# Optimization experiments

Hardware: AMD Instinct MI355X
Metric: run time of the kernel (lower is better)

The kernel has to match this reference:

```python
import jax, jax.numpy as jnp
import numpy as np

N_NODES = 100000
N_EDGES = 1_600_000
IN_C, HID_C, CLS_C = 128, 256, 64


def setup_inputs() -> dict:
    key = jax.random.key(0)
    ks = jax.random.split(key, 8)
    x = jax.random.normal(ks[0], (N_NODES, IN_C), dtype=jnp.float32)
    edge_index = jax.random.randint(ks[1], (2, N_EDGES), 0, N_NODES, dtype=jnp.int64)
    s1 = 1.0 / np.sqrt(IN_C)
    s2 = 1.0 / np.sqrt(HID_C)
    W1l = jax.random.uniform(ks[2], (IN_C, HID_C), jnp.float32, -s1, s1)
    W1r = jax.random.uniform(ks[3], (IN_C, HID_C), jnp.float32, -s1, s1)
    b1 = jnp.zeros((HID_C,), jnp.float32)
    W2l = jax.random.uniform(ks[4], (HID_C, CLS_C), jnp.float32, -s2, s2)
    W2r = jax.random.uniform(ks[5], (HID_C, CLS_C), jnp.float32, -s2, s2)
    b2 = jnp.zeros((CLS_C,), jnp.float32)
    return {"x": x, "edge_index": edge_index,
            "W1l": W1l, "W1r": W1r, "b1": b1,
            "W2l": W2l, "W2r": W2r, "b2": b2}


def _sage_conv(x, src, dst, Wl, Wr, b, num_nodes):
    # mean aggregation of source features onto destination nodes
    agg = jax.ops.segment_sum(x[src], dst, num_segments=num_nodes)  # [N, F]
    deg = jax.ops.segment_sum(jnp.ones((src.shape[0], 1), x.dtype), dst,
                              num_segments=num_nodes)               # [N, 1]
    agg = agg / jnp.maximum(deg, 1.0)  # zero-degree nodes -> 0
    return agg @ Wl + x @ Wr + b


def reference(x, edge_index, W1l, W1r, b1, W2l, W2r, b2):
    src, dst = edge_index[0], edge_index[1]
    n = x.shape[0]
    h = jax.nn.relu(_sage_conv(x, src, dst, W1l, W1r, b1, n))
    # dropout(p=0.5) is identity in eval mode
    out = _sage_conv(h, src, dst, W2l, W2r, b2, n)
    return jax.nn.sigmoid(out)
```

## Files before the change

kernel.cpp:

```cpp
#include <hip/hip_runtime.h>

typedef __attribute__((ext_vector_type(8))) short short8;
typedef __attribute__((ext_vector_type(4))) float floatx4;
typedef __attribute__((ext_vector_type(2))) float floatx2;

static __device__ __forceinline__ unsigned short f2bf(float f) {
  unsigned int u = __builtin_bit_cast(unsigned int, f);
  u += 0x7FFFu + ((u >> 16) & 1u);
  return (unsigned short)(u >> 16);
}
static __device__ __forceinline__ float bf2f(unsigned short s) {
  unsigned int u = ((unsigned int)s) << 16;
  return __builtin_bit_cast(float, u);
}
static __device__ __forceinline__ unsigned int pk4_fp8(float a, float b, float c, float d) {
  int lo = __builtin_amdgcn_cvt_pk_fp8_f32(a, b, 0, false);
  int hi = __builtin_amdgcn_cvt_pk_fp8_f32(c, d, 0, false);
  return (unsigned int)((lo & 0xffff) | ((hi & 0xffff) << 16));
}
static __device__ __forceinline__ floatx4 unpk4_fp8(unsigned int p) {
  floatx2 lo = __builtin_amdgcn_cvt_pk_f32_fp8((int)p, false);
  floatx2 hi = __builtin_amdgcn_cvt_pk_f32_fp8((int)p, true);
  floatx4 r = {lo.x, lo.y, hi.x, hi.y};
  return r;
}

#define NBUCK 512
#define BIN_CHUNK 8192


__global__ __launch_bounds__(256) void bhist(const int* __restrict__ dst,
                                             int* __restrict__ bcnt, int E) {
  __shared__ int h[NBUCK];
  for (int i = threadIdx.x; i < NBUCK; i += 256) h[i] = 0;
  __syncthreads();
  int stride = gridDim.x * 256;
  for (int i = blockIdx.x * 256 + threadIdx.x; i < E; i += stride)
    atomicAdd(&h[dst[i] >> 8], 1);
  __syncthreads();
  for (int i = threadIdx.x; i < NBUCK; i += 256)
    if (h[i]) atomicAdd(&bcnt[i], h[i]);
}

__global__ __launch_bounds__(256) void bscan(const int* __restrict__ bcnt,
                                             int* __restrict__ bbase,
                                             int* __restrict__ bcur,
                                             int* __restrict__ rs, int N, int E) {
  __shared__ int ps[256];
  int t = threadIdx.x;
  int v0 = bcnt[2 * t], v1 = bcnt[2 * t + 1];
  int tsum = v0 + v1;
  ps[t] = tsum;
  __syncthreads();
  for (int off = 1; off < 256; off <<= 1) {
    int x = (t >= off) ? ps[t - off] : 0;
    __syncthreads();
    ps[t] += x;
    __syncthreads();
  }
  int excl = ps[t] - tsum;
  bbase[2 * t] = excl;     bcur[2 * t] = excl;
  bbase[2 * t + 1] = excl + v0; bcur[2 * t + 1] = excl + v0;
  if (t == 0) rs[N] = E;
}

__global__ __launch_bounds__(256) void binscatter(const int* __restrict__ src,
                                                  const int* __restrict__ dst,
                                                  int* __restrict__ bcur,
                                                  unsigned int* __restrict__ staging,
                                                  int E) {
  __shared__ int h[NBUCK];
  __shared__ int cur[NBUCK];
  for (int i = threadIdx.x; i < NBUCK; i += 256) h[i] = 0;
  __syncthreads();
  int base = blockIdx.x * BIN_CHUNK;
  int end = base + BIN_CHUNK; if (end > E) end = E;
  for (int i = base + threadIdx.x; i < end; i += 256)
    atomicAdd(&h[dst[i] >> 8], 1);
  __syncthreads();
  for (int i = threadIdx.x; i < NBUCK; i += 256)
    cur[i] = h[i] ? atomicAdd(&bcur[i], h[i]) : 0;
  __syncthreads();
  for (int i = base + threadIdx.x; i < end; i += 256) {
    int d = dst[i], s = src[i];
    int b = d >> 8;
    int pos = atomicAdd(&cur[b], 1);
    staging[pos] = ((unsigned int)(d & 255) << 17) | (unsigned int)s;
  }
}

__global__ __launch_bounds__(256) void bucketfinal(const unsigned int* __restrict__ staging,
                                                   const int* __restrict__ bbase,
                                                   const int* __restrict__ bcnt,
                                                   int* __restrict__ rs,
                                                   int* __restrict__ csr_src, int N) {
  int b = blockIdx.x;
  int base = bbase[b], cnt = bcnt[b];
  __shared__ int h[256];
  __shared__ int ps[256];
  __shared__ int cur[256];
  int t = threadIdx.x;
  h[t] = 0;
  __syncthreads();
  for (int i = t; i < cnt; i += 256)
    atomicAdd(&h[staging[base + i] >> 17], 1);
  __syncthreads();
  int hv = h[t];
  ps[t] = hv;
  __syncthreads();
  for (int off = 1; off < 256; off <<= 1) {
    int x = (t >= off) ? ps[t - off] : 0;
    __syncthreads();
    ps[t] += x;
    __syncthreads();
  }
  int run = base + ps[t] - hv;
  int w = (b << 8) + t;
  cur[t] = run;
  if (w < N) rs[w] = run;
  __syncthreads();
  for (int i = t; i < cnt; i += 256) {
    unsigned int v = staging[base + i];
    int pos = atomicAdd(&cur[v >> 17], 1);
    csr_src[pos] = (int)(v & 0x1FFFFu);
  }
}

__global__ void convw(const float* __restrict__ W1l, const float* __restrict__ W1r,
                      const float* __restrict__ W2l, const float* __restrict__ W2r,
                      unsigned short* __restrict__ W1p, unsigned short* __restrict__ W2p) {
  int i = blockIdx.x * blockDim.x + threadIdx.x;
  if (i < 8192) {
    int lane = i & 63, ni = (i >> 6) & 3, kk = (i >> 8) & 7, w = i >> 11;
    int fm = lane & 15, fq = lane >> 4;
    int n = w * 64 + ni * 16 + fm;
    int k0 = kk * 32 + fq * 8;
    unsigned short r[8];
#pragma unroll
    for (int j = 0; j < 8; j++) {
      int k = k0 + j;
      float v = (k < 128) ? W1l[k * 256 + n] : W1r[(k - 128) * 256 + n];
      r[j] = f2bf(v);
    }
    *reinterpret_cast<uint4*>(W1p + (size_t)i * 8) = *reinterpret_cast<uint4*>(r);
  } else if (i < 8192 + 4096) {
    int j2 = i - 8192;
    int lane = j2 & 63, ni = (j2 >> 6) & 1, kk = (j2 >> 7) & 7, w = j2 >> 10;
    int fm = lane & 15, fq = lane >> 4;
    int n = w * 32 + ni * 16 + fm;
    int k0 = kk * 32 + fq * 8;
    unsigned short r[8];
#pragma unroll
    for (int j = 0; j < 8; j++) {
      int k = k0 + j;
      float v = (n < 64) ? W2l[k * 64 + n] : W2r[k * 64 + (n - 64)];
      r[j] = f2bf(v);
    }
    *reinterpret_cast<uint4*>(W2p + (size_t)j2 * 8) = *reinterpret_cast<uint4*>(r);
  }
}

__global__ void convx(const float* __restrict__ x, unsigned short* __restrict__ A1,
                      unsigned int* __restrict__ xq, int n_nodes) {
  int i = blockIdx.x * blockDim.x + threadIdx.x;
  if (i < n_nodes * 32) {
    int node = i >> 5, c4 = (i & 31) * 4;
    float4 v = *reinterpret_cast<const float4*>(x + (size_t)node * 128 + c4);
    unsigned short r[4] = { f2bf(v.x), f2bf(v.y), f2bf(v.z), f2bf(v.w) };
    *reinterpret_cast<uint2*>(A1 + (size_t)node * 256 + 128 + c4) =
        *reinterpret_cast<uint2*>(r);
    xq[node * 32 + (i & 31)] = pk4_fp8(v.x, v.y, v.z, v.w);
  }
}

__global__ __launch_bounds__(256) void agg1_kernel(const int* __restrict__ csr_src,
                                                   const int* __restrict__ rs,
                                                   const uint4* __restrict__ xq,
                                                   unsigned short* __restrict__ A1,
                                                   int n_nodes) {
  int lane = threadIdx.x & 63;
  int wave = threadIdx.x >> 6;
  int grp = lane >> 3;
  int ch4 = lane & 7;
  int w = blockIdx.x * 32 + wave * 8 + grp;
  if (w >= n_nodes) return;
  int e0 = rs[w], e1 = rs[w + 1];
  floatx4 a0[4] = {{0,0,0,0},{0,0,0,0},{0,0,0,0},{0,0,0,0}};
  floatx4 a1[4] = {{0,0,0,0},{0,0,0,0},{0,0,0,0},{0,0,0,0}};
  int e = e0;
  for (; e + 1 < e1; e += 2) {
    uint4 p0 = xq[(csr_src[e] << 3) | ch4];
    uint4 p1 = xq[(csr_src[e + 1] << 3) | ch4];
    a0[0] += unpk4_fp8(p0.x); a0[1] += unpk4_fp8(p0.y);
    a0[2] += unpk4_fp8(p0.z); a0[3] += unpk4_fp8(p0.w);
    a1[0] += unpk4_fp8(p1.x); a1[1] += unpk4_fp8(p1.y);
    a1[2] += unpk4_fp8(p1.z); a1[3] += unpk4_fp8(p1.w);
  }
  if (e < e1) {
    uint4 p = xq[(csr_src[e] << 3) | ch4];
    a0[0] += unpk4_fp8(p.x); a0[1] += unpk4_fp8(p.y);
    a0[2] += unpk4_fp8(p.z); a0[3] += unpk4_fp8(p.w);
  }
  int d = e1 - e0; if (d < 1) d = 1;
  float sc = 1.0f / (float)d;
  unsigned short r[16];
#pragma unroll
  for (int j = 0; j < 4; j++) {
    floatx4 a = a0[j] + a1[j];
    r[4 * j + 0] = f2bf(a.x * sc); r[4 * j + 1] = f2bf(a.y * sc);
    r[4 * j + 2] = f2bf(a.z * sc); r[4 * j + 3] = f2bf(a.w * sc);
  }
  unsigned short* dst = A1 + (size_t)w * 256 + ch4 * 16;
  *reinterpret_cast<uint4*>(dst) = *reinterpret_cast<uint4*>(r);
  *reinterpret_cast<uint4*>(dst + 8) = *reinterpret_cast<uint4*>(r + 8);
}

#define LDSW 264
__global__ __launch_bounds__(256, 4) void gemm_fused(const unsigned short* __restrict__ A1,
                                                     const unsigned short* __restrict__ W1p,
                                                     const unsigned short* __restrict__ W2p,
                                                     const float* __restrict__ b1,
                                                     unsigned char* __restrict__ zq,
                                                     unsigned short* __restrict__ rb,
                                                     int M) {
  __shared__ unsigned short smem[64 * LDSW];
  const int tid = threadIdx.x;
  const int lane = tid & 63;
  const int wave = tid >> 6;
  const int m0 = blockIdx.x * 64;
  const int fm = lane & 15;
  const int fq = lane >> 4;
  const short8* __restrict__ W1v = reinterpret_cast<const short8*>(W1p);
  const short8* __restrict__ W2v = reinterpret_cast<const short8*>(W2p);

#pragma unroll
  for (int j = 0; j < 8; j++) {
    int c = j * 256 + tid;
    int row = c >> 5, ch = c & 31;
    int gr = m0 + row; if (gr >= M) gr = M - 1;
    int4 v = *reinterpret_cast<const int4*>(A1 + (size_t)gr * 256 + ch * 8);
    *reinterpret_cast<int4*>(&smem[row * LDSW + ch * 8]) = v;
  }

  float bb[4];
#pragma unroll
  for (int ni = 0; ni < 4; ni++) bb[ni] = b1[wave * 64 + ni * 16 + fm];

  __syncthreads();

  floatx4 acc1[4][4] = {};
#pragma unroll 2
  for (int kk = 0; kk < 8; kk++) {
    short8 af[4], bfr[4];
#pragma unroll
    for (int mi = 0; mi < 4; mi++)
      af[mi] = *reinterpret_cast<const short8*>(
          &smem[(mi * 16 + fm) * LDSW + kk * 32 + fq * 8]);
#pragma unroll
    for (int ni = 0; ni < 4; ni++)
      bfr[ni] = W1v[((wave * 8 + kk) * 4 + ni) * 64 + lane];
#pragma unroll
    for (int mi = 0; mi < 4; mi++)
#pragma unroll
      for (int ni = 0; ni < 4; ni++)
        acc1[mi][ni] = __builtin_amdgcn_mfma_f32_16x16x32_bf16(af[mi], bfr[ni],
                                                               acc1[mi][ni], 0, 0, 0);
  }

  __syncthreads();

#pragma unroll
  for (int mi = 0; mi < 4; mi++)
#pragma unroll
    for (int ni = 0; ni < 4; ni++)
#pragma unroll
      for (int r = 0; r < 4; r++) {
        float v = acc1[mi][ni][r] + bb[ni];
        v = v > 0.f ? v : 0.f;
        smem[(mi * 16 + fq * 4 + r) * LDSW + wave * 64 + ni * 16 + fm] = f2bf(v);
      }
  __syncthreads();

  floatx4 acc2[4][2] = {};
#pragma unroll 2
  for (int kk = 0; kk < 8; kk++) {
    short8 hf[4], wf[2];
#pragma unroll
    for (int mi = 0; mi < 4; mi++)
      hf[mi] = *reinterpret_cast<const short8*>(
          &smem[(mi * 16 + fm) * LDSW + kk * 32 + fq * 8]);
#pragma unroll
    for (int ni = 0; ni < 2; ni++)
      wf[ni] = W2v[((wave * 8 + kk) * 2 + ni) * 64 + lane];
#pragma unroll
    for (int mi = 0; mi < 4; mi++)
#pragma unroll
      for (int ni = 0; ni < 2; ni++)
        acc2[mi][ni] = __builtin_amdgcn_mfma_f32_16x16x32_bf16(hf[mi], wf[ni],
                                                               acc2[mi][ni], 0, 0, 0);
  }

#pragma unroll
  for (int mi = 0; mi < 4; mi++)
#pragma unroll
    for (int ni = 0; ni < 2; ni++)
#pragma unroll
      for (int r = 0; r < 4; r++) {
        int grow = m0 + mi * 16 + fq * 4 + r;
        if (grow < M) {
          float v = acc2[mi][ni][r];
          int col = (wave & 1) * 32 + ni * 16 + fm;
          if (wave < 2) {
            int b8 = __builtin_amdgcn_cvt_pk_fp8_f32(v, v, 0, false);
            zq[grow * 64 + col] = (unsigned char)(b8 & 0xff);
          } else {
            rb[grow * 64 + col] = f2bf(v);
          }
        }
      }
}

__global__ __launch_bounds__(256) void agg2_final(const uint4* __restrict__ zq,
                                                  const unsigned short* __restrict__ rb,
                                                  const int* __restrict__ csr_src,
                                                  const int* __restrict__ rs,
                                                  const float* __restrict__ b2,
                                                  float* __restrict__ out, int n_nodes) {
  int lane = threadIdx.x & 63;
  int wave = threadIdx.x >> 6;
  int grp = lane >> 2;
  int ch = lane & 3;
  int w = blockIdx.x * 64 + wave * 16 + grp;
  if (w >= n_nodes) return;
  int e0 = rs[w], e1 = rs[w + 1];
  floatx4 a0[4] = {{0,0,0,0},{0,0,0,0},{0,0,0,0},{0,0,0,0}};
  floatx4 a1[4] = {{0,0,0,0},{0,0,0,0},{0,0,0,0},{0,0,0,0}};
  int e = e0;
  for (; e + 1 < e1; e += 2) {
    uint4 p0 = zq[(csr_src[e] << 2) | ch];
    uint4 p1 = zq[(csr_src[e + 1] << 2) | ch];
    a0[0] += unpk4_fp8(p0.x); a0[1] += unpk4_fp8(p0.y);
    a0[2] += unpk4_fp8(p0.z); a0[3] += unpk4_fp8(p0.w);
    a1[0] += unpk4_fp8(p1.x); a1[1] += unpk4_fp8(p1.y);
    a1[2] += unpk4_fp8(p1.z); a1[3] += unpk4_fp8(p1.w);
  }
  if (e < e1) {
    uint4 p = zq[(csr_src[e] << 2) | ch];
    a0[0] += unpk4_fp8(p.x); a0[1] += unpk4_fp8(p.y);
    a0[2] += unpk4_fp8(p.z); a0[3] += unpk4_fp8(p.w);
  }
  int d = e1 - e0; if (d < 1) d = 1;
  float sc = 1.0f / (float)d;
  const unsigned short* rbp = rb + w * 64 + ch * 16;
  const float* b2p = b2 + ch * 16;
  float* op = out + (size_t)w * 64 + ch * 16;
#pragma unroll
  for (int j = 0; j < 4; j++) {
    floatx4 a = a0[j] + a1[j];
    uint2 rr = *reinterpret_cast<const uint2*>(rbp + 4 * j);
    float4 bv = *reinterpret_cast<const float4*>(b2p + 4 * j);
    float r0 = bf2f((unsigned short)(rr.x & 0xffff));
    float r1 = bf2f((unsigned short)(rr.x >> 16));
    float r2 = bf2f((unsigned short)(rr.y & 0xffff));
    float r3 = bf2f((unsigned short)(rr.y >> 16));
    float4 o;
    o.x = 1.0f / (1.0f + __expf(-(a.x * sc + r0 + bv.x)));
    o.y = 1.0f / (1.0f + __expf(-(a.y * sc + r1 + bv.y)));
    o.z = 1.0f / (1.0f + __expf(-(a.z * sc + r2 + bv.z)));
    o.w = 1.0f / (1.0f + __expf(-(a.w * sc + r3 + bv.w)));
    *reinterpret_cast<float4*>(op + 4 * j) = o;
  }
}

extern "C" void kernel_launch(void* const* d_in, const int* in_sizes, int n_in,
                              void* d_out, int out_size, void* d_ws, size_t ws_size,
                              hipStream_t stream) {
  const float* x   = (const float*)d_in[0];
  const int*   ei  = (const int*)d_in[1];
  const float* W1l = (const float*)d_in[2];
  const float* W1r = (const float*)d_in[3];
  const float* b1  = (const float*)d_in[4];
  const float* W2l = (const float*)d_in[5];
  const float* W2r = (const float*)d_in[6];
  const float* b2  = (const float*)d_in[7];
  float* out = (float*)d_out;

  const int N = in_sizes[0] / 128;
  const int E = in_sizes[1] / 2;
  const int* src = ei;
  const int* dst = ei + E;

  char* wsb = (char*)d_ws;
  size_t off = 0;
  auto alloc = [&](size_t bytes) -> void* {
    void* p = wsb + off;
    off += (bytes + 511) & ~(size_t)511;
    return p;
  };
  int* rs       = (int*)alloc((size_t)(N + 1) * 4);
  int* csr_src  = (int*)alloc((size_t)E * 4 + 64);
  int* bcnt     = (int*)alloc(NBUCK * 4);
  int* bbase    = (int*)alloc(NBUCK * 4);
  int* bcur     = (int*)alloc(NBUCK * 4);
  unsigned int* staging = (unsigned int*)alloc((size_t)E * 4);
  unsigned short* W1p = (unsigned short*)alloc(256 * 256 * 2);
  unsigned short* W2p = (unsigned short*)alloc(128 * 256 * 2);
  unsigned short* A1  = (unsigned short*)alloc((size_t)N * 256 * 2);
  unsigned int* xq    = (unsigned int*)alloc((size_t)N * 128);
  unsigned char* zq   = (unsigned char*)alloc((size_t)N * 64);
  unsigned short* rb  = (unsigned short*)alloc((size_t)N * 64 * 2);
  (void)ws_size; (void)n_in; (void)out_size;

  const int nbuckReal = (N + 255) / 256;
  const int nchunks = (E + BIN_CHUNK - 1) / BIN_CHUNK;

  hipMemsetAsync(bcnt, 0, NBUCK * 4, stream);
  bhist<<<256, 256, 0, stream>>>(dst, bcnt, E);
  bscan<<<1, 256, 0, stream>>>(bcnt, bbase, bcur, rs, N, E);
  binscatter<<<nchunks, 256, 0, stream>>>(src, dst, bcur, staging, E);
  bucketfinal<<<nbuckReal, 256, 0, stream>>>(staging, bbase, bcnt, rs, csr_src, N);

  convw<<<(8192 + 4096 + 255) / 256, 256, 0, stream>>>(W1l, W1r, W2l, W2r, W1p, W2p);
  convx<<<(N * 32 + 255) / 256, 256, 0, stream>>>(x, A1, xq, N);

  agg1_kernel<<<(N + 31) / 32, 256, 0, stream>>>(csr_src, rs, (const uint4*)xq, A1, N);

  gemm_fused<<<(N + 63) / 64, 256, 0, stream>>>(A1, W1p, W2p, b1, zq, rb, N);

  agg2_final<<<(N + 63) / 64, 256, 0, stream>>>((const uint4*)zq, rb, csr_src, rs, b2, out, N);
}
```

Baseline: 260.5 us.

## Fuse layer-1 neighbor aggregation into GEMM kernel, dropping A1 intermediate buffer

Removes the separate agg1 kernel and the bf16 A1 staging buffer. The GEMM kernel now gathers fp8 neighbor features per row directly into shared memory and converts x to bf16 itself before the MFMA loop. This avoids writing and re-reading a 51 MB intermediate and saves a launch. The cost is that the latency-bound gather now runs inside a GEMM kernel whose occupancy is limited by launch bounds and LDS use, and it cannot overlap with that kernel's compute.

```diff
diff --git a/kernel.cpp b/kernel.cpp
--- a/kernel.cpp
+++ b/kernel.cpp
@@ -160,63 +160,21 @@
   }
 }
 
-__global__ void convx(const float* __restrict__ x, unsigned short* __restrict__ A1,
-                      unsigned int* __restrict__ xq, int n_nodes) {
+__global__ void convx(const float* __restrict__ x, unsigned int* __restrict__ xq,
+                      int n_nodes) {
   int i = blockIdx.x * blockDim.x + threadIdx.x;
   if (i < n_nodes * 32) {
     int node = i >> 5, c4 = (i & 31) * 4;
     float4 v = *reinterpret_cast<const float4*>(x + (size_t)node * 128 + c4);
-    unsigned short r[4] = { f2bf(v.x), f2bf(v.y), f2bf(v.z), f2bf(v.w) };
-    *reinterpret_cast<uint2*>(A1 + (size_t)node * 256 + 128 + c4) =
-        *reinterpret_cast<uint2*>(r);
-    xq[node * 32 + (i & 31)] = pk4_fp8(v.x, v.y, v.z, v.w);
-  }
-}
-
-__global__ __launch_bounds__(256) void agg1_kernel(const int* __restrict__ csr_src,
-                                                   const int* __restrict__ rs,
-                                                   const uint4* __restrict__ xq,
-                                                   unsigned short* __restrict__ A1,
-                                                   int n_nodes) {
-  int lane = threadIdx.x & 63;
-  int wave = threadIdx.x >> 6;
-  int grp = lane >> 3;
-  int ch4 = lane & 7;
-  int w = blockIdx.x * 32 + wave * 8 + grp;
-  if (w >= n_nodes) return;
-  int e0 = rs[w], e1 = rs[w + 1];
-  floatx4 a0[4] = {{0,0,0,0},{0,0,0,0},{0,0,0,0},{0,0,0,0}};
-  floatx4 a1[4] = {{0,0,0,0},{0,0,0,0},{0,0,0,0},{0,0,0,0}};
-  int e = e0;
-  for (; e + 1 < e1; e += 2) {
-    uint4 p0 = xq[(csr_src[e] << 3) | ch4];
-    uint4 p1 = xq[(csr_src[e + 1] << 3) | ch4];
-    a0[0] += unpk4_fp8(p0.x); a0[1] += unpk4_fp8(p0.y);
-    a0[2] += unpk4_fp8(p0.z); a0[3] += unpk4_fp8(p0.w);
-    a1[0] += unpk4_fp8(p1.x); a1[1] += unpk4_fp8(p1.y);
-    a1[2] += unpk4_fp8(p1.z); a1[3] += unpk4_fp8(p1.w);
-  }
-  if (e < e1) {
-    uint4 p = xq[(csr_src[e] << 3) | ch4];
-    a0[0] += unpk4_fp8(p.x); a0[1] += unpk4_fp8(p.y);
-    a0[2] += unpk4_fp8(p.z); a0[3] += unpk4_fp8(p.w);
-  }
-  int d = e1 - e0; if (d < 1) d = 1;
-  float sc = 1.0f / (float)d;
-  unsigned short r[16];
-#pragma unroll
-  for (int j = 0; j < 4; j++) {
-    floatx4 a = a0[j] + a1[j];
-    r[4 * j + 0] = f2bf(a.x * sc); r[4 * j + 1] = f2bf(a.y * sc);
-    r[4 * j + 2] = f2bf(a.z * sc); r[4 * j + 3] = f2bf(a.w * sc);
-  }
-  unsigned short* dst = A1 + (size_t)w * 256 + ch4 * 16;
-  *reinterpret_cast<uint4*>(dst) = *reinterpret_cast<uint4*>(r);
-  *reinterpret_cast<uint4*>(dst + 8) = *reinterpret_cast<uint4*>(r + 8);
+    xq[i] = pk4_fp8(v.x, v.y, v.z, v.w);
+  }
 }
 
 #define LDSW 264
-__global__ __launch_bounds__(256, 4) void gemm_fused(const unsigned short* __restrict__ A1,
+__global__ __launch_bounds__(256, 4) void gemm_fused(const float* __restrict__ x,
+                                                     const uint4* __restrict__ xq,
+                                                     const int* __restrict__ csr_src,
+                                                     const int* __restrict__ rs,
                                                      const unsigned short* __restrict__ W1p,
                                                      const unsigned short* __restrict__ W2p,
                                                      const float* __restrict__ b1,
@@ -236,10 +194,53 @@
 #pragma unroll
   for (int j = 0; j < 8; j++) {
     int c = j * 256 + tid;
-    int row = c >> 5, ch = c & 31;
+    int row = c >> 5, f4 = c & 31;
     int gr = m0 + row; if (gr >= M) gr = M - 1;
-    int4 v = *reinterpret_cast<const int4*>(A1 + (size_t)gr * 256 + ch * 8);
-    *reinterpret_cast<int4*>(&smem[row * LDSW + ch * 8]) = v;
+    float4 v = *reinterpret_cast<const float4*>(x + (size_t)gr * 128 + f4 * 4);
+    unsigned short r[4] = { f2bf(v.x), f2bf(v.y), f2bf(v.z), f2bf(v.w) };
+    *reinterpret_cast<uint2*>(&smem[row * LDSW + 128 + f4 * 4]) =
+        *reinterpret_cast<uint2*>(r);
+  }
+
+  {
+    const int grp = lane >> 3;
+    const int ch4 = lane & 7;
+#pragma unroll
+    for (int p = 0; p < 2; p++) {
+      int row = p * 32 + wave * 8 + grp;
+      int w = m0 + row;
+      if (w < M) {
+        int e0 = rs[w], e1 = rs[w + 1];
+        floatx4 a0[4] = {{0,0,0,0},{0,0,0,0},{0,0,0,0},{0,0,0,0}};
+        floatx4 a1[4] = {{0,0,0,0},{0,0,0,0},{0,0,0,0},{0,0,0,0}};
+        int e = e0;
+        for (; e + 1 < e1; e += 2) {
+          uint4 p0 = xq[(csr_src[e] << 3) | ch4];
+          uint4 p1 = xq[(csr_src[e + 1] << 3) | ch4];
+          a0[0] += unpk4_fp8(p0.x); a0[1] += unpk4_fp8(p0.y);
+          a0[2] += unpk4_fp8(p0.z); a0[3] += unpk4_fp8(p0.w);
+          a1[0] += unpk4_fp8(p1.x); a1[1] += unpk4_fp8(p1.y);
+          a1[2] += unpk4_fp8(p1.z); a1[3] += unpk4_fp8(p1.w);
+        }
+        if (e < e1) {
+          uint4 pv = xq[(csr_src[e] << 3) | ch4];
+          a0[0] += unpk4_fp8(pv.x); a0[1] += unpk4_fp8(pv.y);
+          a0[2] += unpk4_fp8(pv.z); a0[3] += unpk4_fp8(pv.w);
+        }
+        int d = e1 - e0; if (d < 1) d = 1;
+        float sc = 1.0f / (float)d;
+        unsigned short r[16];
+#pragma unroll
+        for (int j = 0; j < 4; j++) {
+          floatx4 a = a0[j] + a1[j];
+          r[4 * j + 0] = f2bf(a.x * sc); r[4 * j + 1] = f2bf(a.y * sc);
+          r[4 * j + 2] = f2bf(a.z * sc); r[4 * j + 3] = f2bf(a.w * sc);
+        }
+        unsigned short* dstp = &smem[row * LDSW + ch4 * 16];
+        *reinterpret_cast<uint4*>(dstp) = *reinterpret_cast<uint4*>(r);
+        *reinterpret_cast<uint4*>(dstp + 8) = *reinterpret_cast<uint4*>(r + 8);
+      }
+    }
   }
 
   float bb[4];
@@ -405,7 +406,6 @@
   unsigned int* staging = (unsigned int*)alloc((size_t)E * 4);
   unsigned short* W1p = (unsigned short*)alloc(256 * 256 * 2);
   unsigned short* W2p = (unsigned short*)alloc(128 * 256 * 2);
-  unsigned short* A1  = (unsigned short*)alloc((size_t)N * 256 * 2);
   unsigned int* xq    = (unsigned int*)alloc((size_t)N * 128);
   unsigned char* zq   = (unsigned char*)alloc((size_t)N * 64);
   unsigned short* rb  = (unsigned short*)alloc((size_t)N * 64 * 2);
@@ -421,11 +421,10 @@
   bucketfinal<<<nbuckReal, 256, 0, stream>>>(staging, bbase, bcnt, rs, csr_src, N);
 
   convw<<<(8192 + 4096 + 255) / 256, 256, 0, stream>>>(W1l, W1r, W2l, W2r, W1p, W2p);
-  convx<<<(N * 32 + 255) / 256, 256, 0, stream>>>(x, A1, xq, N);
-
-  agg1_kernel<<<(N + 31) / 32, 256, 0, stream>>>(csr_src, rs, (const uint4*)xq, A1, N);
-
-  gemm_fused<<<(N + 63) / 64, 256, 0, stream>>>(A1, W1p, W2p, b1, zq, rb, N);
+  convx<<<(N * 32 + 255) / 256, 256, 0, stream>>>(x, xq, N);
+
+  gemm_fused<<<(N + 63) / 64, 256, 0, stream>>>(x, (const uint4*)xq, csr_src, rs,
+                                                W1p, W2p, b1, zq, rb, N);
 
   agg2_final<<<(N + 63) / 64, 256, 0, stream>>>((const uint4*)zq, rb, csr_src, rs, b2, out, N);
 }
```

New measurement: 259.0 us. Within noise of the previous version (-0.6%).
